# Kernel optimization log

Measured on AMD Instinct MI355X. Metric: run time of the kernel, lower is better.

## Reference

```python
import jax, jax.numpy as jnp
import numpy as np

N, E, D, ED, G = 50000, 600000, 128, 32, 64
NEG_SLOPE = 0.2

def layer_norm(x, g, b, eps=1e-5):
    mu = jnp.mean(x, axis=-1, keepdims=True)
    var = jnp.var(x, axis=-1, keepdims=True)
    return (x - mu) * jax.lax.rsqrt(var + eps) * g + b

def eagat(x, src, dst, edge_attr, W, a_src, a_dst, We, a_e, bias):
    # GATConv with edge features, heads=1; messages flow src -> dst
    xl = x @ W                               # [N, D]
    ee = edge_attr @ We                      # [E, D]
    al_s = xl @ a_src                        # [N]
    al_d = xl @ a_dst                        # [N]
    e = jax.nn.leaky_relu(al_s[src] + al_d[dst] + ee @ a_e, NEG_SLOPE)  # [E]
    # segment softmax over incoming edges of each dst node
    m = jax.ops.segment_max(e, dst, num_segments=N)
    ex = jnp.exp(e - m[dst])
    s = jax.ops.segment_sum(ex, dst, num_segments=N)
    alpha = ex / (s[dst] + 1e-16)            # [E]
    out = jax.ops.segment_sum(xl[src] * alpha[:, None], dst, num_segments=N)
    return out + bias

def setup_inputs() -> dict:
    key = jax.random.key(0)
    ks = jax.random.split(key, 24)
    p = lambda k, shp, sc=0.1: jax.random.normal(k, shp, dtype=jnp.float32) * sc
    inp = {
        "x": jax.random.normal(ks[0], (N, D), dtype=jnp.float32),
        "edge_attr": jax.random.normal(ks[1], (E, ED), dtype=jnp.float32),
        "W1": p(ks[2], (D, D)), "as1": p(ks[3], (D,)), "ad1": p(ks[4], (D,)),
        "We1": p(ks[5], (ED, D)), "ae1": p(ks[6], (D,)), "b1": jnp.zeros((D,), jnp.float32),
        "g1": jnp.ones((D,), jnp.float32), "be1": jnp.zeros((D,), jnp.float32),
        "W2": p(ks[7], (D, D)), "as2": p(ks[8], (D,)), "ad2": p(ks[9], (D,)),
        "We2": p(ks[10], (ED, D)), "ae2": p(ks[11], (D,)), "b2": jnp.zeros((D,), jnp.float32),
        "g2": jnp.ones((D,), jnp.float32), "be2": jnp.zeros((D,), jnp.float32),
        "Wl": p(ks[12], (D, D)), "bl": jnp.zeros((D,), jnp.float32),
        "gl": jnp.ones((D,), jnp.float32), "bel": jnp.zeros((D,), jnp.float32),
        "edge_index": jax.random.randint(ks[13], (2, E), 0, N, dtype=jnp.int64),
        "batch": jnp.sort(jax.random.randint(ks[14], (N,), 0, G, dtype=jnp.int64)),
    }
    return inp

def reference(x, edge_attr, W1, as1, ad1, We1, ae1, b1, g1, be1,
              W2, as2, ad2, We2, ae2, b2, g2, be2, Wl, bl, gl, bel,
              edge_index, batch):
    src, dst = edge_index[0], edge_index[1]
    x1 = eagat(x, src, dst, edge_attr, W1, as1, ad1, We1, ae1, b1)
    x2 = layer_norm(x1, g1, be1)
    x3 = eagat(x2, src, dst, edge_attr, W2, as2, ad2, We2, ae2, b2)
    x4 = layer_norm(x3, g2, be2)
    # global mean pool over graphs
    sums = jax.ops.segment_sum(x4, batch, num_segments=G)          # [G, D]
    cnt = jax.ops.segment_sum(jnp.ones((x4.shape[0],), x4.dtype), batch, num_segments=G)
    pooled = sums / jnp.maximum(cnt, 1.0)[:, None]
    out = jax.nn.relu(layer_norm(pooled @ Wl + bl, gl, bel))
    return out
```

## Files before the change

### kernel.cpp

```cpp
#include <hip/hip_runtime.h>
#include <math.h>


typedef __attribute__((ext_vector_type(8))) short bf16x8;
typedef __attribute__((ext_vector_type(4))) float f32x4;

static __device__ __forceinline__ unsigned short f2bf(float f) {
    unsigned u = __float_as_uint(f);
    unsigned r = (u + 0x7fff + ((u >> 16) & 1)) >> 16;
    return (unsigned short)r;
}
static __device__ __forceinline__ float bf2f_lo(unsigned u) { return __uint_as_float(u << 16); }
static __device__ __forceinline__ float bf2f_hi(unsigned u) { return __uint_as_float(u & 0xffff0000u); }

__global__ __launch_bounds__(256) void prep_weights(
    const float* __restrict__ W1, const float* __restrict__ W2,
    const float* __restrict__ We1, const float* __restrict__ ae1,
    const float* __restrict__ We2, const float* __restrict__ ae2,
    unsigned short* __restrict__ W1bT, unsigned short* __restrict__ W2bT,
    float* __restrict__ wa, int4* __restrict__ counts4, int nc4,
    int4* __restrict__ pooled4, int np4, int zc)
{
    int b = blockIdx.x, t = threadIdx.x;
    if (b < 64) {
        int i = b * 256 + t;
        int k = i >> 7, n = i & 127;
        W1bT[n * 128 + k] = f2bf(W1[i]);
        W2bT[n * 128 + k] = f2bf(W2[i]);
    } else if (b == 64) {
        int o = t >> 2;
        int qq = t & 3;
        const float* We = (o < 32) ? We1 : We2;
        const float* ae = (o < 32) ? ae1 : ae2;
        int r = o & 31;
        const float4* Wr = (const float4*)(We + r * 128 + qq * 32);
        const float4* ar = (const float4*)(ae + qq * 32);
        float s = 0.f;
#pragma unroll
        for (int c4 = 0; c4 < 8; c4++) {
            float4 wv = Wr[c4]; float4 av = ar[c4];
            s += wv.x*av.x + wv.y*av.y + wv.z*av.z + wv.w*av.w;
        }
        s += __shfl_xor(s, 1); s += __shfl_xor(s, 2);
        if (qq == 0) wa[o] = s;
    } else if (b < 65 + zc) {
        int i = (b - 65) * 256 + t;
        if (i < nc4) counts4[i] = (int4){0, 0, 0, 0};
    } else {
        int i = (b - 65 - zc) * 256 + t;
        if (i < np4) pooled4[i] = (int4){0, 0, 0, 0};
    }
}

__global__ __launch_bounds__(256) void edge_dots_count(
    const float* __restrict__ ea, const float* __restrict__ wa,
    const int* __restrict__ srcv, const int* __restrict__ dstv,
    int* __restrict__ counts, int2* __restrict__ payload, int E)
{
    int j = blockIdx.x * 256 + threadIdx.x;
    if (j >= E) return;
    int dst = dstv[j];
    int src = srcv[j];
    int r = atomicAdd(&counts[dst << 4], 1);

    const float4* e4 = (const float4*)(ea + (size_t)j * 32);
    float4 v[8];
#pragma unroll
    for (int i = 0; i < 8; i++) v[i] = e4[i];

    float s1 = 0.f, s2 = 0.f;
#pragma unroll
    for (int i = 0; i < 8; i++) {
        float4 w1 = ((const float4*)wa)[i];
        float4 w2 = ((const float4*)(wa + 32))[i];
        s1 += v[i].x*w1.x + v[i].y*w1.y + v[i].z*w1.z + v[i].w*w1.w;
        s2 += v[i].x*w2.x + v[i].y*w2.y + v[i].z*w2.z + v[i].w*w2.w;
    }
    if (r < 64) {
        unsigned pe = ((unsigned)f2bf(s1) << 16) | (unsigned)f2bf(s2);
        int2 pv;
        pv.x = src;
        pv.y = (int)pe;
        payload[((size_t)dst << 6) + r] = pv;
    }
}

template<bool BF16IN>
__global__ __launch_bounds__(256) void gemm_mfma(
    const void* __restrict__ Xv, const unsigned short* __restrict__ WbT,
    const float* __restrict__ asrc, const float* __restrict__ adst,
    unsigned short* __restrict__ XLb, float* __restrict__ als, float* __restrict__ ald,
    int nrows)
{
    __shared__ unsigned short tile[64][136];
    int t = threadIdx.x;
    int wave = t >> 6;
    int lane = t & 63;
    int l = lane & 15, q = lane >> 4;
    int row0 = blockIdx.x * 64 + wave * 16;

    int arow = row0 + l;
    bool avalid = arow < nrows;

    f32x4 acc[8];
#pragma unroll
    for (int c = 0; c < 8; c++) acc[c] = (f32x4){0.f, 0.f, 0.f, 0.f};

#pragma unroll
    for (int kt = 0; kt < 4; kt++) {
        bf16x8 afrag;
        if (avalid) {
            if constexpr (BF16IN) {
                const unsigned short* xrow = (const unsigned short*)Xv + (size_t)arow * 128 + q * 8;
                afrag = *(const bf16x8*)(xrow + kt * 32);
            } else {
                const float* xrow = (const float*)Xv + (size_t)arow * 128 + q * 8;
                float4 v0 = *(const float4*)(xrow + kt * 32);
                float4 v1 = *(const float4*)(xrow + kt * 32 + 4);
                afrag[0] = (short)f2bf(v0.x); afrag[1] = (short)f2bf(v0.y);
                afrag[2] = (short)f2bf(v0.z); afrag[3] = (short)f2bf(v0.w);
                afrag[4] = (short)f2bf(v1.x); afrag[5] = (short)f2bf(v1.y);
                afrag[6] = (short)f2bf(v1.z); afrag[7] = (short)f2bf(v1.w);
            }
        } else {
#pragma unroll
            for (int j = 0; j < 8; j++) afrag[j] = 0;
        }
#pragma unroll
        for (int c = 0; c < 8; c++) {
            bf16x8 bfrag = *(const bf16x8*)(WbT + (((c * 16 + l) << 7) + kt * 32 + q * 8));
            acc[c] = __builtin_amdgcn_mfma_f32_16x16x32_bf16(afrag, bfrag, acc[c], 0, 0, 0);
        }
    }

    float as_[8], ad_[8];
#pragma unroll
    for (int c = 0; c < 8; c++) { as_[c] = asrc[c * 16 + l]; ad_[c] = adst[c * 16 + l]; }

#pragma unroll
    for (int r = 0; r < 4; r++) {
        int row = row0 + q * 4 + r;
        bool valid = row < nrows;
        float ps = 0.f, pd = 0.f;
#pragma unroll
        for (int c = 0; c < 8; c++) {
            float v = acc[c][r];
            ps += v * as_[c]; pd += v * ad_[c];
        }
#pragma unroll
        for (int o = 8; o >= 1; o >>= 1) { ps += __shfl_xor(ps, o); pd += __shfl_xor(pd, o); }
        if (l == 0 && valid) { als[row] = ps; ald[row] = pd; }
    }

#pragma unroll
    for (int c = 0; c < 8; c++) {
#pragma unroll
        for (int r = 0; r < 4; r++) {
            unsigned u = (unsigned)f2bf(acc[c][r]);
            unsigned up = (unsigned)__shfl_xor((int)u, 1);
            if (!(lane & 1)) {
                *(unsigned*)&tile[wave * 16 + q * 4 + r][c * 16 + l] = u | (up << 16);
            }
        }
    }
    __syncthreads();

    int base = blockIdx.x * 64;
#pragma unroll
    for (int it = 0; it < 4; it++) {
        int row = it * 16 + (t >> 4);
        int seg = t & 15;
        if (base + row < nrows) {
            bf16x8 vv = *(const bf16x8*)&tile[row][seg * 8];
            *(bf16x8*)(XLb + (size_t)(base + row) * 128 + seg * 8) = vv;
        }
    }
}

template<int EOFF>
__global__ __launch_bounds__(256) void aggregate_ln(
    const unsigned short* __restrict__ XLb, const int2* __restrict__ payload,
    const int* __restrict__ counts,
    const float* __restrict__ als, const float* __restrict__ ald,
    const float* __restrict__ bias, const float* __restrict__ gamma, const float* __restrict__ beta,
    unsigned short* __restrict__ XoutB, int N)
{
    int node = blockIdx.x * 4 + (threadIdx.x >> 6);
    if (node >= N) return;
    int lane = threadIdx.x & 63;
    int deg = counts[node << 4];
    if (deg > 64) deg = 64;
    float ald_n = ald[node];

    const unsigned* rows = (const unsigned*)XLb;

    float w_mine = 0.f;
    int   s_mine = 0;
    if (lane < deg) {
        int2 pv = payload[((size_t)node << 6) + lane];
        s_mine = pv.x;
        unsigned ue = (unsigned)pv.y;
        float ed = (EOFF == 1) ? bf2f_hi(ue) : bf2f_lo(ue);
        float e = ed + als[s_mine] + ald_n;
        e = (e >= 0.f) ? e : 0.2f * e;
        w_mine = __expf(fminf(e, 60.f));
    }

    float ssum = w_mine;
#pragma unroll
    for (int o = 32; o >= 1; o >>= 1) ssum += __shfl_xor(ssum, o);

    float acc0 = 0.f, acc1 = 0.f;
    int j = 0;
    for (; j + 8 <= deg; j += 8) {
        int s0=__shfl(s_mine,j),   s1=__shfl(s_mine,j+1), s2=__shfl(s_mine,j+2), s3=__shfl(s_mine,j+3);
        int s4=__shfl(s_mine,j+4), s5=__shfl(s_mine,j+5), s6=__shfl(s_mine,j+6), s7=__shfl(s_mine,j+7);
        unsigned u0 = rows[((size_t)s0 << 6) + lane];
        unsigned u1 = rows[((size_t)s1 << 6) + lane];
        unsigned u2 = rows[((size_t)s2 << 6) + lane];
        unsigned u3 = rows[((size_t)s3 << 6) + lane];
        unsigned u4 = rows[((size_t)s4 << 6) + lane];
        unsigned u5 = rows[((size_t)s5 << 6) + lane];
        unsigned u6 = rows[((size_t)s6 << 6) + lane];
        unsigned u7 = rows[((size_t)s7 << 6) + lane];
        float w0=__shfl(w_mine,j),   w1=__shfl(w_mine,j+1), w2=__shfl(w_mine,j+2), w3=__shfl(w_mine,j+3);
        float w4=__shfl(w_mine,j+4), w5=__shfl(w_mine,j+5), w6=__shfl(w_mine,j+6), w7=__shfl(w_mine,j+7);
        acc0 += w0*bf2f_lo(u0); acc1 += w0*bf2f_hi(u0);
        acc0 += w1*bf2f_lo(u1); acc1 += w1*bf2f_hi(u1);
        acc0 += w2*bf2f_lo(u2); acc1 += w2*bf2f_hi(u2);
        acc0 += w3*bf2f_lo(u3); acc1 += w3*bf2f_hi(u3);
        acc0 += w4*bf2f_lo(u4); acc1 += w4*bf2f_hi(u4);
        acc0 += w5*bf2f_lo(u5); acc1 += w5*bf2f_hi(u5);
        acc0 += w6*bf2f_lo(u6); acc1 += w6*bf2f_hi(u6);
        acc0 += w7*bf2f_lo(u7); acc1 += w7*bf2f_hi(u7);
    }
    for (; j + 4 <= deg; j += 4) {
        int s0=__shfl(s_mine,j), s1=__shfl(s_mine,j+1), s2=__shfl(s_mine,j+2), s3=__shfl(s_mine,j+3);
        unsigned u0 = rows[((size_t)s0 << 6) + lane];
        unsigned u1 = rows[((size_t)s1 << 6) + lane];
        unsigned u2 = rows[((size_t)s2 << 6) + lane];
        unsigned u3 = rows[((size_t)s3 << 6) + lane];
        float w0=__shfl(w_mine,j), w1=__shfl(w_mine,j+1), w2=__shfl(w_mine,j+2), w3=__shfl(w_mine,j+3);
        acc0 += w0*bf2f_lo(u0); acc1 += w0*bf2f_hi(u0);
        acc0 += w1*bf2f_lo(u1); acc1 += w1*bf2f_hi(u1);
        acc0 += w2*bf2f_lo(u2); acc1 += w2*bf2f_hi(u2);
        acc0 += w3*bf2f_lo(u3); acc1 += w3*bf2f_hi(u3);
    }
    for (; j < deg; j++) {
        int s0 = __shfl(s_mine, j);
        float w0 = __shfl(w_mine, j);
        unsigned u0 = rows[((size_t)s0 << 6) + lane];
        acc0 += w0*bf2f_lo(u0); acc1 += w0*bf2f_hi(u0);
    }

    float2 bi = *(const float2*)(bias + 2 * lane);
    float inv = 1.f / (ssum + 1e-16f);
    float y0 = acc0 * inv + bi.x;
    float y1 = acc1 * inv + bi.y;

    float s = y0 + y1;
#pragma unroll
    for (int o = 32; o >= 1; o >>= 1) s += __shfl_xor(s, o);
    float mean = s * (1.f / 128.f);
    float d0 = y0 - mean, d1 = y1 - mean;
    float v = d0 * d0 + d1 * d1;
#pragma unroll
    for (int o = 32; o >= 1; o >>= 1) v += __shfl_xor(v, o);
    float r = rsqrtf(v * (1.f / 128.f) + 1e-5f);
    float2 ga = *(const float2*)(gamma + 2 * lane);
    float2 be = *(const float2*)(beta  + 2 * lane);
    float o0 = d0 * r * ga.x + be.x;
    float o1 = d1 * r * ga.y + be.y;
    unsigned packed = (unsigned)f2bf(o0) | ((unsigned)f2bf(o1) << 16);
    ((unsigned*)XoutB)[((size_t)node << 6) + lane] = packed;
}

__global__ __launch_bounds__(64) void pool_partial(
    const unsigned* __restrict__ XAb4, const int* __restrict__ batch,
    float* __restrict__ pooled, int n)
{
    int chunk0 = blockIdx.x * 32;
    if (chunk0 >= n) return;
    int t = threadIdx.x;
    int end = min(chunk0 + 32, n);
    float a0 = 0.f, a1 = 0.f;
    int gcur = batch[chunk0];
    for (int r = chunk0; r < end; r++) {
        int g = batch[r];
        if (g != gcur) {
            atomicAdd(&pooled[gcur * 128 + 2 * t],     a0);
            atomicAdd(&pooled[gcur * 128 + 2 * t + 1], a1);
            a0 = 0.f; a1 = 0.f; gcur = g;
        }
        unsigned u = XAb4[((size_t)r << 6) + t];
        a0 += bf2f_lo(u); a1 += bf2f_hi(u);
    }
    atomicAdd(&pooled[gcur * 128 + 2 * t],     a0);
    atomicAdd(&pooled[gcur * 128 + 2 * t + 1], a1);
}

__global__ __launch_bounds__(128) void pool_head(
    const float* __restrict__ pooled, const int* __restrict__ batch,
    const float* __restrict__ Wl, const float* __restrict__ bl,
    const float* __restrict__ gl, const float* __restrict__ bel,
    float* __restrict__ out, int n)
{
    int g = blockIdx.x, t = threadIdx.x;
    int lo = 0, hi = n;
    while (lo < hi) { int mid = (lo + hi) >> 1; if (batch[mid] < g) lo = mid + 1; else hi = mid; }
    int s0 = lo;
    hi = n;
    while (lo < hi) { int mid = (lo + hi) >> 1; if (batch[mid] < g + 1) lo = mid + 1; else hi = mid; }
    float cntf = (float)(lo - s0);

    __shared__ float ps[128];
    __shared__ float xr[4];
    ps[t] = pooled[g * 128 + t] / fmaxf(cntf, 1.f);
    __syncthreads();

    float y = bl[t];
#pragma unroll 4
    for (int k = 0; k < 128; k++) y += ps[k] * Wl[k * 128 + t];

    float s = y;
#pragma unroll
    for (int o = 32; o >= 1; o >>= 1) s += __shfl_xor(s, o);
    if ((t & 63) == 0) xr[t >> 6] = s;
    __syncthreads();
    float mean = (xr[0] + xr[1]) * (1.f / 128.f);
    float d = y - mean;
    float v = d * d;
#pragma unroll
    for (int o = 32; o >= 1; o >>= 1) v += __shfl_xor(v, o);
    if ((t & 63) == 0) xr[2 + (t >> 6)] = v;
    __syncthreads();
    float var = (xr[2] + xr[3]) * (1.f / 128.f);
    float z = d * rsqrtf(var + 1e-5f) * gl[t] + bel[t];
    out[g * 128 + t] = fmaxf(z, 0.f);
}


extern "C" void kernel_launch(void* const* d_in, const int* in_sizes, int n_in,
                              void* d_out, int out_size, void* d_ws, size_t ws_size,
                              hipStream_t stream)
{
    const float* x    = (const float*)d_in[0];
    const float* ea   = (const float*)d_in[1];
    const float* W1   = (const float*)d_in[2];
    const float* as1  = (const float*)d_in[3];
    const float* ad1  = (const float*)d_in[4];
    const float* We1  = (const float*)d_in[5];
    const float* ae1  = (const float*)d_in[6];
    const float* b1   = (const float*)d_in[7];
    const float* g1   = (const float*)d_in[8];
    const float* be1  = (const float*)d_in[9];
    const float* W2   = (const float*)d_in[10];
    const float* as2  = (const float*)d_in[11];
    const float* ad2  = (const float*)d_in[12];
    const float* We2  = (const float*)d_in[13];
    const float* ae2  = (const float*)d_in[14];
    const float* b2   = (const float*)d_in[15];
    const float* g2   = (const float*)d_in[16];
    const float* be2  = (const float*)d_in[17];
    const float* Wlin = (const float*)d_in[18];
    const float* bl   = (const float*)d_in[19];
    const float* gl   = (const float*)d_in[20];
    const float* bel  = (const float*)d_in[21];
    const int*   ei   = (const int*)d_in[22];
    const int*   batch= (const int*)d_in[23];
    float* out = (float*)d_out;

    int N = in_sizes[0] / 128;
    int E = in_sizes[1] / 32;
    int G = out_size / 128;
    const int* srcv = ei;
    const int* dstv = ei + E;

    char* wsb = (char*)d_ws;
    size_t off = 0;
    auto alloc = [&](size_t bytes) -> void* {
        void* p = wsb + off;
        off += (bytes + 15) & ~(size_t)15;
        return p;
    };
    unsigned short* XLb  = (unsigned short*)alloc((size_t)N * 128 * 2);
    unsigned short* XAb  = (unsigned short*)alloc((size_t)N * 128 * 2);
    unsigned short* W1bT = (unsigned short*)alloc(16384 * 2);
    unsigned short* W2bT = (unsigned short*)alloc(16384 * 2);
    int2*  payload= (int2*)alloc((size_t)N * 64 * 8);
    float* als    = (float*)alloc((size_t)N * 4);
    float* ald    = (float*)alloc((size_t)N * 4);
    float* wa     = (float*)alloc(64 * 4);
    float* pooled = (float*)alloc((size_t)G * 128 * 4);
    int*   counts = (int*)alloc((size_t)N * 64);

    int egrid = (E + 255) / 256;
    int mgrid = (N + 63) / 64;
    int agrid = (N + 3) / 4;
    int pgrid = (N + 31) / 32;

    int nc4 = N * 4;
    int np4 = (G * 128) / 4;
    int zc = (nc4 + 255) / 256;
    int zp = (np4 + 255) / 256;
    prep_weights<<<65 + zc + zp, 256, 0, stream>>>(
        W1, W2, We1, ae1, We2, ae2, W1bT, W2bT, wa,
        (int4*)counts, nc4, (int4*)pooled, np4, zc);

    edge_dots_count<<<egrid, 256, 0, stream>>>(ea, wa, srcv, dstv, counts, payload, E);

    gemm_mfma<false><<<mgrid, 256, 0, stream>>>(x, W1bT, as1, ad1, XLb, als, ald, N);
    aggregate_ln<1><<<agrid, 256, 0, stream>>>(XLb, payload, counts, als, ald, b1, g1, be1, XAb, N);

    gemm_mfma<true><<<mgrid, 256, 0, stream>>>(XAb, W2bT, as2, ad2, XLb, als, ald, N);
    aggregate_ln<2><<<agrid, 256, 0, stream>>>(XLb, payload, counts, als, ald, b2, g2, be2, XAb, N);

    pool_partial<<<pgrid, 64, 0, stream>>>((const unsigned*)XAb, batch, pooled, N);
    pool_head<<<G, 128, 0, stream>>>(pooled, batch, Wlin, bl, gl, bel, out, N);
}
```

Measured before the change: 344.9 us.

## Fuse edge-dot/bucketing kernel with first GEMM and compact degree counters

Merges the edge attention-dot and dst-bucketing kernel with the first-layer node GEMM into one launch, with blocks split by index between the two jobs so they run concurrently and one launch is saved. Degree counters are shrunk from one per 64-byte line to a dense int array, cutting the zeroing traffic at the cost of more atomic contention on shared cache lines. Payload writes become 64-bit nontemporal stores to avoid polluting cache. The fused kernel carries the GEMM's shared-memory tile even for edge blocks, which can reduce occupancy.

New measurement: 351.7 us. No clear change (+2.0%).

```diff
diff --git a/kernel.cpp b/kernel.cpp
--- a/kernel.cpp
+++ b/kernel.cpp
@@ -52,42 +52,127 @@
     }
 }
 
-__global__ __launch_bounds__(256) void edge_dots_count(
+__global__ __launch_bounds__(256) void edge_gemm1(
     const float* __restrict__ ea, const float* __restrict__ wa,
     const int* __restrict__ srcv, const int* __restrict__ dstv,
-    int* __restrict__ counts, int2* __restrict__ payload, int E)
-{
-    int j = blockIdx.x * 256 + threadIdx.x;
-    if (j >= E) return;
-    int dst = dstv[j];
-    int src = srcv[j];
-    int r = atomicAdd(&counts[dst << 4], 1);
-
-    const float4* e4 = (const float4*)(ea + (size_t)j * 32);
-    float4 v[8];
-#pragma unroll
-    for (int i = 0; i < 8; i++) v[i] = e4[i];
-
-    float s1 = 0.f, s2 = 0.f;
-#pragma unroll
-    for (int i = 0; i < 8; i++) {
-        float4 w1 = ((const float4*)wa)[i];
-        float4 w2 = ((const float4*)(wa + 32))[i];
-        s1 += v[i].x*w1.x + v[i].y*w1.y + v[i].z*w1.z + v[i].w*w1.w;
-        s2 += v[i].x*w2.x + v[i].y*w2.y + v[i].z*w2.z + v[i].w*w2.w;
-    }
-    if (r < 64) {
-        unsigned pe = ((unsigned)f2bf(s1) << 16) | (unsigned)f2bf(s2);
-        int2 pv;
-        pv.x = src;
-        pv.y = (int)pe;
-        payload[((size_t)dst << 6) + r] = pv;
-    }
-}
-
-template<bool BF16IN>
-__global__ __launch_bounds__(256) void gemm_mfma(
-    const void* __restrict__ Xv, const unsigned short* __restrict__ WbT,
+    int* __restrict__ counts, unsigned long long* __restrict__ payload, int E, int eg,
+    const float* __restrict__ Xv, const unsigned short* __restrict__ WbT,
+    const float* __restrict__ asrc, const float* __restrict__ adst,
+    unsigned short* __restrict__ XLb, float* __restrict__ als, float* __restrict__ ald,
+    int nrows)
+{
+    int t = threadIdx.x;
+    if (blockIdx.x < eg) {
+        int j = blockIdx.x * 256 + t;
+        if (j >= E) return;
+        int dst = dstv[j];
+        int src = srcv[j];
+        int r = atomicAdd(&counts[dst], 1);
+
+        const float4* e4 = (const float4*)(ea + (size_t)j * 32);
+        float4 v[8];
+#pragma unroll
+        for (int i = 0; i < 8; i++) v[i] = e4[i];
+
+        float s1 = 0.f, s2 = 0.f;
+#pragma unroll
+        for (int i = 0; i < 8; i++) {
+            float4 w1 = ((const float4*)wa)[i];
+            float4 w2 = ((const float4*)(wa + 32))[i];
+            s1 += v[i].x*w1.x + v[i].y*w1.y + v[i].z*w1.z + v[i].w*w1.w;
+            s2 += v[i].x*w2.x + v[i].y*w2.y + v[i].z*w2.z + v[i].w*w2.w;
+        }
+        if (r < 64) {
+            unsigned pe = ((unsigned)f2bf(s1) << 16) | (unsigned)f2bf(s2);
+            unsigned long long pv = (unsigned long long)(unsigned)src
+                                  | ((unsigned long long)pe << 32);
+            __builtin_nontemporal_store(pv, &payload[((size_t)dst << 6) + r]);
+        }
+        return;
+    }
+
+    __shared__ unsigned short tile[64][136];
+    int bid = blockIdx.x - eg;
+    int wave = t >> 6;
+    int lane = t & 63;
+    int l = lane & 15, q = lane >> 4;
+    int row0 = bid * 64 + wave * 16;
+
+    int arow = row0 + l;
+    bool avalid = arow < nrows;
+
+    f32x4 acc[8];
+#pragma unroll
+    for (int c = 0; c < 8; c++) acc[c] = (f32x4){0.f, 0.f, 0.f, 0.f};
+
+#pragma unroll
+    for (int kt = 0; kt < 4; kt++) {
+        bf16x8 afrag;
+        if (avalid) {
+            const float* xrow = Xv + (size_t)arow * 128 + q * 8;
+            float4 v0 = *(const float4*)(xrow + kt * 32);
+            float4 v1 = *(const float4*)(xrow + kt * 32 + 4);
+            afrag[0] = (short)f2bf(v0.x); afrag[1] = (short)f2bf(v0.y);
+            afrag[2] = (short)f2bf(v0.z); afrag[3] = (short)f2bf(v0.w);
+            afrag[4] = (short)f2bf(v1.x); afrag[5] = (short)f2bf(v1.y);
+            afrag[6] = (short)f2bf(v1.z); afrag[7] = (short)f2bf(v1.w);
+        } else {
+#pragma unroll
+            for (int jj = 0; jj < 8; jj++) afrag[jj] = 0;
+        }
+#pragma unroll
+        for (int c = 0; c < 8; c++) {
+            bf16x8 bfrag = *(const bf16x8*)(WbT + (((c * 16 + l) << 7) + kt * 32 + q * 8));
+            acc[c] = __builtin_amdgcn_mfma_f32_16x16x32_bf16(afrag, bfrag, acc[c], 0, 0, 0);
+        }
+    }
+
+    float as_[8], ad_[8];
+#pragma unroll
+    for (int c = 0; c < 8; c++) { as_[c] = asrc[c * 16 + l]; ad_[c] = adst[c * 16 + l]; }
+
+#pragma unroll
+    for (int r = 0; r < 4; r++) {
+        int row = row0 + q * 4 + r;
+        bool valid = row < nrows;
+        float ps = 0.f, pd = 0.f;
+#pragma unroll
+        for (int c = 0; c < 8; c++) {
+            float v = acc[c][r];
+            ps += v * as_[c]; pd += v * ad_[c];
+        }
+#pragma unroll
+        for (int o = 8; o >= 1; o >>= 1) { ps += __shfl_xor(ps, o); pd += __shfl_xor(pd, o); }
+        if (l == 0 && valid) { als[row] = ps; ald[row] = pd; }
+    }
+
+#pragma unroll
+    for (int c = 0; c < 8; c++) {
+#pragma unroll
+        for (int r = 0; r < 4; r++) {
+            unsigned u = (unsigned)f2bf(acc[c][r]);
+            unsigned up = (unsigned)__shfl_xor((int)u, 1);
+            if (!(lane & 1)) {
+                *(unsigned*)&tile[wave * 16 + q * 4 + r][c * 16 + l] = u | (up << 16);
+            }
+        }
+    }
+    __syncthreads();
+
+    int base = bid * 64;
+#pragma unroll
+    for (int it = 0; it < 4; it++) {
+        int row = it * 16 + (t >> 4);
+        int seg = t & 15;
+        if (base + row < nrows) {
+            bf16x8 vv = *(const bf16x8*)&tile[row][seg * 8];
+            *(bf16x8*)(XLb + (size_t)(base + row) * 128 + seg * 8) = vv;
+        }
+    }
+}
+
+__global__ __launch_bounds__(256) void gemm_mfma_bf16(
+    const unsigned short* __restrict__ Xv, const unsigned short* __restrict__ WbT,
     const float* __restrict__ asrc, const float* __restrict__ adst,
     unsigned short* __restrict__ XLb, float* __restrict__ als, float* __restrict__ ald,
     int nrows)
@@ -110,21 +195,11 @@
     for (int kt = 0; kt < 4; kt++) {
         bf16x8 afrag;
         if (avalid) {
-            if constexpr (BF16IN) {
-                const unsigned short* xrow = (const unsigned short*)Xv + (size_t)arow * 128 + q * 8;
-                afrag = *(const bf16x8*)(xrow + kt * 32);
-            } else {
-                const float* xrow = (const float*)Xv + (size_t)arow * 128 + q * 8;
-                float4 v0 = *(const float4*)(xrow + kt * 32);
-                float4 v1 = *(const float4*)(xrow + kt * 32 + 4);
-                afrag[0] = (short)f2bf(v0.x); afrag[1] = (short)f2bf(v0.y);
-                afrag[2] = (short)f2bf(v0.z); afrag[3] = (short)f2bf(v0.w);
-                afrag[4] = (short)f2bf(v1.x); afrag[5] = (short)f2bf(v1.y);
-                afrag[6] = (short)f2bf(v1.z); afrag[7] = (short)f2bf(v1.w);
-            }
+            const unsigned short* xrow = Xv + (size_t)arow * 128 + q * 8;
+            afrag = *(const bf16x8*)(xrow + kt * 32);
         } else {
 #pragma unroll
-            for (int j = 0; j < 8; j++) afrag[j] = 0;
+            for (int jj = 0; jj < 8; jj++) afrag[jj] = 0;
         }
 #pragma unroll
         for (int c = 0; c < 8; c++) {
@@ -179,7 +254,7 @@
 
 template<int EOFF>
 __global__ __launch_bounds__(256) void aggregate_ln(
-    const unsigned short* __restrict__ XLb, const int2* __restrict__ payload,
+    const unsigned short* __restrict__ XLb, const unsigned long long* __restrict__ payload,
     const int* __restrict__ counts,
     const float* __restrict__ als, const float* __restrict__ ald,
     const float* __restrict__ bias, const float* __restrict__ gamma, const float* __restrict__ beta,
@@ -188,7 +263,7 @@
     int node = blockIdx.x * 4 + (threadIdx.x >> 6);
     if (node >= N) return;
     int lane = threadIdx.x & 63;
-    int deg = counts[node << 4];
+    int deg = counts[node];
     if (deg > 64) deg = 64;
     float ald_n = ald[node];
 
@@ -197,9 +272,9 @@
     float w_mine = 0.f;
     int   s_mine = 0;
     if (lane < deg) {
-        int2 pv = payload[((size_t)node << 6) + lane];
-        s_mine = pv.x;
-        unsigned ue = (unsigned)pv.y;
+        unsigned long long pv = payload[((size_t)node << 6) + lane];
+        s_mine = (int)(unsigned)pv;
+        unsigned ue = (unsigned)(pv >> 32);
         float ed = (EOFF == 1) ? bf2f_hi(ue) : bf2f_lo(ue);
         float e = ed + als[s_mine] + ald_n;
         e = (e >= 0.f) ? e : 0.2f * e;
@@ -387,19 +462,19 @@
     unsigned short* XAb  = (unsigned short*)alloc((size_t)N * 128 * 2);
     unsigned short* W1bT = (unsigned short*)alloc(16384 * 2);
     unsigned short* W2bT = (unsigned short*)alloc(16384 * 2);
-    int2*  payload= (int2*)alloc((size_t)N * 64 * 8);
+    unsigned long long* payload = (unsigned long long*)alloc((size_t)N * 64 * 8);
     float* als    = (float*)alloc((size_t)N * 4);
     float* ald    = (float*)alloc((size_t)N * 4);
     float* wa     = (float*)alloc(64 * 4);
     float* pooled = (float*)alloc((size_t)G * 128 * 4);
-    int*   counts = (int*)alloc((size_t)N * 64);
+    int*   counts = (int*)alloc((size_t)N * 4);
 
     int egrid = (E + 255) / 256;
     int mgrid = (N + 63) / 64;
     int agrid = (N + 3) / 4;
     int pgrid = (N + 31) / 32;
 
-    int nc4 = N * 4;
+    int nc4 = N / 4 + (N % 4 != 0);
     int np4 = (G * 128) / 4;
     int zc = (nc4 + 255) / 256;
     int zp = (np4 + 255) / 256;
@@ -407,12 +482,13 @@
         W1, W2, We1, ae1, We2, ae2, W1bT, W2bT, wa,
         (int4*)counts, nc4, (int4*)pooled, np4, zc);
 
-    edge_dots_count<<<egrid, 256, 0, stream>>>(ea, wa, srcv, dstv, counts, payload, E);
-
-    gemm_mfma<false><<<mgrid, 256, 0, stream>>>(x, W1bT, as1, ad1, XLb, als, ald, N);
+    edge_gemm1<<<egrid + mgrid, 256, 0, stream>>>(
+        ea, wa, srcv, dstv, counts, payload, E, egrid,
+        x, W1bT, as1, ad1, XLb, als, ald, N);
+
     aggregate_ln<1><<<agrid, 256, 0, stream>>>(XLb, payload, counts, als, ald, b1, g1, be1, XAb, N);
 
-    gemm_mfma<true><<<mgrid, 256, 0, stream>>>(XAb, W2bT, as2, ad2, XLb, als, ald, N);
+    gemm_mfma_bf16<<<mgrid, 256, 0, stream>>>(XAb, W2bT, as2, ad2, XLb, als, ald, N);
     aggregate_ln<2><<<agrid, 256, 0, stream>>>(XLb, payload, counts, als, ald, b2, g2, be2, XAb, N);
 
     pool_partial<<<pgrid, 64, 0, stream>>>((const unsigned*)XAb, batch, pooled, N);
```

## Replace padded per-node edge slots with compact CSR via count-scan-scatter

Applied to the files above, without the earlier changes.

Edge bucketing moves from fixed 64-slot padded arrays per destination to a compact CSR layout. Edge dots and counts are computed first, a single-block prefix scan builds offsets, and a scatter pass places the packed src/dot pairs contiguously. The aggregate kernels then read from the offsets. This shrinks the payload buffer and the counts zeroing and improves locality for the gathers, but it adds two launches, including a serial single-block scan over 50k nodes, and a second pass over the edges.

After: 443.5 us. +28.6%, slower.

```diff
diff --git a/kernel.cpp b/kernel.cpp
--- a/kernel.cpp
+++ b/kernel.cpp
@@ -52,37 +52,74 @@
     }
 }
 
-__global__ __launch_bounds__(256) void edge_dots_count(
+__global__ __launch_bounds__(256) void edge_dots(
     const float* __restrict__ ea, const float* __restrict__ wa,
-    const int* __restrict__ srcv, const int* __restrict__ dstv,
-    int* __restrict__ counts, int2* __restrict__ payload, int E)
+    const int* __restrict__ dstv,
+    int* __restrict__ counts, unsigned* __restrict__ dots, int E)
 {
     int j = blockIdx.x * 256 + threadIdx.x;
     if (j >= E) return;
-    int dst = dstv[j];
-    int src = srcv[j];
-    int r = atomicAdd(&counts[dst << 4], 1);
-
-    const float4* e4 = (const float4*)(ea + (size_t)j * 32);
-    float4 v[8];
-#pragma unroll
-    for (int i = 0; i < 8; i++) v[i] = e4[i];
+    int dst = __builtin_nontemporal_load(&dstv[j]);
+    atomicAdd(&counts[dst], 1);
+
+    const f32x4* e4 = (const f32x4*)(ea + (size_t)j * 32);
+    f32x4 v[8];
+#pragma unroll
+    for (int i = 0; i < 8; i++) v[i] = __builtin_nontemporal_load(&e4[i]);
 
     float s1 = 0.f, s2 = 0.f;
 #pragma unroll
     for (int i = 0; i < 8; i++) {
         float4 w1 = ((const float4*)wa)[i];
         float4 w2 = ((const float4*)(wa + 32))[i];
-        s1 += v[i].x*w1.x + v[i].y*w1.y + v[i].z*w1.z + v[i].w*w1.w;
-        s2 += v[i].x*w2.x + v[i].y*w2.y + v[i].z*w2.z + v[i].w*w2.w;
-    }
-    if (r < 64) {
-        unsigned pe = ((unsigned)f2bf(s1) << 16) | (unsigned)f2bf(s2);
-        int2 pv;
-        pv.x = src;
-        pv.y = (int)pe;
-        payload[((size_t)dst << 6) + r] = pv;
-    }
+        s1 += v[i][0]*w1.x + v[i][1]*w1.y + v[i][2]*w1.z + v[i][3]*w1.w;
+        s2 += v[i][0]*w2.x + v[i][1]*w2.y + v[i][2]*w2.z + v[i][3]*w2.w;
+    }
+    unsigned pe = ((unsigned)f2bf(s1) << 16) | (unsigned)f2bf(s2);
+    __builtin_nontemporal_store(pe, &dots[j]);
+}
+
+__global__ __launch_bounds__(1024) void prefix_scan(
+    const int* __restrict__ counts, int* __restrict__ offs,
+    int* __restrict__ woff, int n)
+{
+    __shared__ int wsum[16];
+    __shared__ int carry_s;
+    int t = threadIdx.x, lane = t & 63, w = t >> 6;
+    if (t == 0) { carry_s = 0; offs[0] = 0; }
+    __syncthreads();
+    for (int base = 0; base < n; base += 1024) {
+        int i = base + t;
+        int c = (i < n) ? counts[i] : 0;
+        int s = c;
+#pragma unroll
+        for (int o = 1; o < 64; o <<= 1) { int v = __shfl_up(s, o); if (lane >= o) s += v; }
+        if (lane == 63) wsum[w] = s;
+        __syncthreads();
+        int prev = 0;
+        for (int k = 0; k < w; k++) prev += wsum[k];
+        int total = prev;
+        for (int k = w; k < 16; k++) total += wsum[k];
+        int excl = carry_s + prev + s - c;
+        if (i < n) { woff[i] = excl; offs[i + 1] = excl + c; }
+        __syncthreads();
+        if (t == 0) carry_s += total;
+        __syncthreads();
+    }
+}
+
+__global__ __launch_bounds__(256) void scatter_pass(
+    const int* __restrict__ srcv, const int* __restrict__ dstv,
+    const unsigned* __restrict__ dots, int* __restrict__ woff,
+    unsigned long long* __restrict__ payload, int E)
+{
+    int j = blockIdx.x * 256 + threadIdx.x;
+    if (j >= E) return;
+    int dst = __builtin_nontemporal_load(&dstv[j]);
+    int src = __builtin_nontemporal_load(&srcv[j]);
+    unsigned d = __builtin_nontemporal_load(&dots[j]);
+    int pos = atomicAdd(&woff[dst], 1);
+    payload[pos] = (unsigned long long)(unsigned)src | ((unsigned long long)d << 32);
 }
 
 template<bool BF16IN>
@@ -124,7 +161,7 @@
             }
         } else {
 #pragma unroll
-            for (int j = 0; j < 8; j++) afrag[j] = 0;
+            for (int jj = 0; jj < 8; jj++) afrag[jj] = 0;
         }
 #pragma unroll
         for (int c = 0; c < 8; c++) {
@@ -179,8 +216,8 @@
 
 template<int EOFF>
 __global__ __launch_bounds__(256) void aggregate_ln(
-    const unsigned short* __restrict__ XLb, const int2* __restrict__ payload,
-    const int* __restrict__ counts,
+    const unsigned short* __restrict__ XLb, const unsigned long long* __restrict__ payload,
+    const int* __restrict__ offs,
     const float* __restrict__ als, const float* __restrict__ ald,
     const float* __restrict__ bias, const float* __restrict__ gamma, const float* __restrict__ beta,
     unsigned short* __restrict__ XoutB, int N)
@@ -188,7 +225,8 @@
     int node = blockIdx.x * 4 + (threadIdx.x >> 6);
     if (node >= N) return;
     int lane = threadIdx.x & 63;
-    int deg = counts[node << 4];
+    int start = offs[node];
+    int deg = offs[node + 1] - start;
     if (deg > 64) deg = 64;
     float ald_n = ald[node];
 
@@ -197,9 +235,9 @@
     float w_mine = 0.f;
     int   s_mine = 0;
     if (lane < deg) {
-        int2 pv = payload[((size_t)node << 6) + lane];
-        s_mine = pv.x;
-        unsigned ue = (unsigned)pv.y;
+        unsigned long long pv = payload[(size_t)start + lane];
+        s_mine = (int)(unsigned)pv;
+        unsigned ue = (unsigned)(pv >> 32);
         float ed = (EOFF == 1) ? bf2f_hi(ue) : bf2f_lo(ue);
         float e = ed + als[s_mine] + ald_n;
         e = (e >= 0.f) ? e : 0.2f * e;
@@ -387,19 +425,22 @@
     unsigned short* XAb  = (unsigned short*)alloc((size_t)N * 128 * 2);
     unsigned short* W1bT = (unsigned short*)alloc(16384 * 2);
     unsigned short* W2bT = (unsigned short*)alloc(16384 * 2);
-    int2*  payload= (int2*)alloc((size_t)N * 64 * 8);
+    unsigned long long* payload = (unsigned long long*)alloc((size_t)E * 8);
+    unsigned* dots  = (unsigned*)alloc((size_t)E * 4);
+    int*   offs   = (int*)alloc((size_t)(N + 1) * 4);
+    int*   woff   = (int*)alloc((size_t)N * 4);
     float* als    = (float*)alloc((size_t)N * 4);
     float* ald    = (float*)alloc((size_t)N * 4);
     float* wa     = (float*)alloc(64 * 4);
     float* pooled = (float*)alloc((size_t)G * 128 * 4);
-    int*   counts = (int*)alloc((size_t)N * 64);
+    int*   counts = (int*)alloc((size_t)N * 4);
 
     int egrid = (E + 255) / 256;
     int mgrid = (N + 63) / 64;
     int agrid = (N + 3) / 4;
     int pgrid = (N + 31) / 32;
 
-    int nc4 = N * 4;
+    int nc4 = (N + 3) / 4;
     int np4 = (G * 128) / 4;
     int zc = (nc4 + 255) / 256;
     int zp = (np4 + 255) / 256;
@@ -407,13 +448,15 @@
         W1, W2, We1, ae1, We2, ae2, W1bT, W2bT, wa,
         (int4*)counts, nc4, (int4*)pooled, np4, zc);
 
-    edge_dots_count<<<egrid, 256, 0, stream>>>(ea, wa, srcv, dstv, counts, payload, E);
+    edge_dots<<<egrid, 256, 0, stream>>>(ea, wa, dstv, counts, dots, E);
+    prefix_scan<<<1, 1024, 0, stream>>>(counts, offs, woff, N);
+    scatter_pass<<<egrid, 256, 0, stream>>>(srcv, dstv, dots, woff, payload, E);
 
     gemm_mfma<false><<<mgrid, 256, 0, stream>>>(x, W1bT, as1, ad1, XLb, als, ald, N);
-    aggregate_ln<1><<<agrid, 256, 0, stream>>>(XLb, payload, counts, als, ald, b1, g1, be1, XAb, N);
+    aggregate_ln<1><<<agrid, 256, 0, stream>>>(XLb, payload, offs, als, ald, b1, g1, be1, XAb, N);
 
     gemm_mfma<true><<<mgrid, 256, 0, stream>>>(XAb, W2bT, as2, ad2, XLb, als, ald, N);
-    aggregate_ln<2><<<agrid, 256, 0, stream>>>(XLb, payload, counts, als, ald, b2, g2, be2, XAb, N);
+    aggregate_ln<2><<<agrid, 256, 0, stream>>>(XLb, payload, offs, als, ald, b2, g2, be2, XAb, N);
 
     pool_partial<<<pgrid, 64, 0, stream>>>((const unsigned*)XAb, batch, pooled, N);
     pool_head<<<G, 128, 0, stream>>>(pooled, batch, Wlin, bl, gl, bel, out, N);
```

## Fuse mean-pool accumulation into second aggregate kernel and compact degree counters

Applied to the files above, without the earlier changes.

Removes the separate pool_partial kernel. The second aggregate_ln now atomically adds each node's normalized row straight into the per-graph pooled buffer, so the bf16 layer-2 output is no longer written and re-read. Degree counters shrink from 64-byte padded slots to packed ints, which cuts zeroing and footprint. Edge inputs are read with nontemporal loads. The risk is heavy float-atomic contention: roughly 780 nodes per graph all add into the same 128 addresses, replacing a kernel that did mostly chunk-local sums. Packed counters may also add cache-line contention between neighbouring nodes.

New measurement: 456.0 us. 1.32x slower.

```diff
diff --git a/kernel.cpp b/kernel.cpp
--- a/kernel.cpp
+++ b/kernel.cpp
@@ -55,32 +55,31 @@
 __global__ __launch_bounds__(256) void edge_dots_count(
     const float* __restrict__ ea, const float* __restrict__ wa,
     const int* __restrict__ srcv, const int* __restrict__ dstv,
-    int* __restrict__ counts, int2* __restrict__ payload, int E)
+    int* __restrict__ counts, unsigned long long* __restrict__ payload, int E)
 {
     int j = blockIdx.x * 256 + threadIdx.x;
     if (j >= E) return;
-    int dst = dstv[j];
-    int src = srcv[j];
-    int r = atomicAdd(&counts[dst << 4], 1);
-
-    const float4* e4 = (const float4*)(ea + (size_t)j * 32);
-    float4 v[8];
-#pragma unroll
-    for (int i = 0; i < 8; i++) v[i] = e4[i];
+    int dst = __builtin_nontemporal_load(&dstv[j]);
+    int src = __builtin_nontemporal_load(&srcv[j]);
+    int r = atomicAdd(&counts[dst], 1);
+
+    const f32x4* e4 = (const f32x4*)(ea + (size_t)j * 32);
+    f32x4 v[8];
+#pragma unroll
+    for (int i = 0; i < 8; i++) v[i] = __builtin_nontemporal_load(&e4[i]);
 
     float s1 = 0.f, s2 = 0.f;
 #pragma unroll
     for (int i = 0; i < 8; i++) {
         float4 w1 = ((const float4*)wa)[i];
         float4 w2 = ((const float4*)(wa + 32))[i];
-        s1 += v[i].x*w1.x + v[i].y*w1.y + v[i].z*w1.z + v[i].w*w1.w;
-        s2 += v[i].x*w2.x + v[i].y*w2.y + v[i].z*w2.z + v[i].w*w2.w;
+        s1 += v[i][0]*w1.x + v[i][1]*w1.y + v[i][2]*w1.z + v[i][3]*w1.w;
+        s2 += v[i][0]*w2.x + v[i][1]*w2.y + v[i][2]*w2.z + v[i][3]*w2.w;
     }
     if (r < 64) {
         unsigned pe = ((unsigned)f2bf(s1) << 16) | (unsigned)f2bf(s2);
-        int2 pv;
-        pv.x = src;
-        pv.y = (int)pe;
+        unsigned long long pv = (unsigned long long)(unsigned)src
+                              | ((unsigned long long)pe << 32);
         payload[((size_t)dst << 6) + r] = pv;
     }
 }
@@ -124,7 +123,7 @@
             }
         } else {
 #pragma unroll
-            for (int j = 0; j < 8; j++) afrag[j] = 0;
+            for (int jj = 0; jj < 8; jj++) afrag[jj] = 0;
         }
 #pragma unroll
         for (int c = 0; c < 8; c++) {
@@ -177,18 +176,19 @@
     }
 }
 
-template<int EOFF>
+template<int EOFF, bool POOL>
 __global__ __launch_bounds__(256) void aggregate_ln(
-    const unsigned short* __restrict__ XLb, const int2* __restrict__ payload,
+    const unsigned short* __restrict__ XLb, const unsigned long long* __restrict__ payload,
     const int* __restrict__ counts,
     const float* __restrict__ als, const float* __restrict__ ald,
     const float* __restrict__ bias, const float* __restrict__ gamma, const float* __restrict__ beta,
-    unsigned short* __restrict__ XoutB, int N)
+    unsigned short* __restrict__ XoutB, const int* __restrict__ batch,
+    float* __restrict__ pooled, int N)
 {
     int node = blockIdx.x * 4 + (threadIdx.x >> 6);
     if (node >= N) return;
     int lane = threadIdx.x & 63;
-    int deg = counts[node << 4];
+    int deg = counts[node];
     if (deg > 64) deg = 64;
     float ald_n = ald[node];
 
@@ -197,9 +197,9 @@
     float w_mine = 0.f;
     int   s_mine = 0;
     if (lane < deg) {
-        int2 pv = payload[((size_t)node << 6) + lane];
-        s_mine = pv.x;
-        unsigned ue = (unsigned)pv.y;
+        unsigned long long pv = payload[((size_t)node << 6) + lane];
+        s_mine = (int)(unsigned)pv;
+        unsigned ue = (unsigned)(pv >> 32);
         float ed = (EOFF == 1) ? bf2f_hi(ue) : bf2f_lo(ue);
         float e = ed + als[s_mine] + ald_n;
         e = (e >= 0.f) ? e : 0.2f * e;
@@ -271,32 +271,14 @@
     float2 be = *(const float2*)(beta  + 2 * lane);
     float o0 = d0 * r * ga.x + be.x;
     float o1 = d1 * r * ga.y + be.y;
-    unsigned packed = (unsigned)f2bf(o0) | ((unsigned)f2bf(o1) << 16);
-    ((unsigned*)XoutB)[((size_t)node << 6) + lane] = packed;
-}
-
-__global__ __launch_bounds__(64) void pool_partial(
-    const unsigned* __restrict__ XAb4, const int* __restrict__ batch,
-    float* __restrict__ pooled, int n)
-{
-    int chunk0 = blockIdx.x * 32;
-    if (chunk0 >= n) return;
-    int t = threadIdx.x;
-    int end = min(chunk0 + 32, n);
-    float a0 = 0.f, a1 = 0.f;
-    int gcur = batch[chunk0];
-    for (int r = chunk0; r < end; r++) {
-        int g = batch[r];
-        if (g != gcur) {
-            atomicAdd(&pooled[gcur * 128 + 2 * t],     a0);
-            atomicAdd(&pooled[gcur * 128 + 2 * t + 1], a1);
-            a0 = 0.f; a1 = 0.f; gcur = g;
-        }
-        unsigned u = XAb4[((size_t)r << 6) + t];
-        a0 += bf2f_lo(u); a1 += bf2f_hi(u);
-    }
-    atomicAdd(&pooled[gcur * 128 + 2 * t],     a0);
-    atomicAdd(&pooled[gcur * 128 + 2 * t + 1], a1);
+    if constexpr (POOL) {
+        int g = batch[node];
+        atomicAdd(&pooled[g * 128 + 2 * lane],     o0);
+        atomicAdd(&pooled[g * 128 + 2 * lane + 1], o1);
+    } else {
+        unsigned packed = (unsigned)f2bf(o0) | ((unsigned)f2bf(o1) << 16);
+        ((unsigned*)XoutB)[((size_t)node << 6) + lane] = packed;
+    }
 }
 
 __global__ __launch_bounds__(128) void pool_head(
@@ -387,19 +369,18 @@
     unsigned short* XAb  = (unsigned short*)alloc((size_t)N * 128 * 2);
     unsigned short* W1bT = (unsigned short*)alloc(16384 * 2);
     unsigned short* W2bT = (unsigned short*)alloc(16384 * 2);
-    int2*  payload= (int2*)alloc((size_t)N * 64 * 8);
+    unsigned long long* payload = (unsigned long long*)alloc((size_t)N * 64 * 8);
     float* als    = (float*)alloc((size_t)N * 4);
     float* ald    = (float*)alloc((size_t)N * 4);
     float* wa     = (float*)alloc(64 * 4);
     float* pooled = (float*)alloc((size_t)G * 128 * 4);
-    int*   counts = (int*)alloc((size_t)N * 64);
+    int*   counts = (int*)alloc((size_t)N * 4);
 
     int egrid = (E + 255) / 256;
     int mgrid = (N + 63) / 64;
     int agrid = (N + 3) / 4;
-    int pgrid = (N + 31) / 32;
-
-    int nc4 = N * 4;
+
+    int nc4 = (N + 3) / 4;
     int np4 = (G * 128) / 4;
     int zc = (nc4 + 255) / 256;
     int zp = (np4 + 255) / 256;
@@ -410,11 +391,12 @@
     edge_dots_count<<<egrid, 256, 0, stream>>>(ea, wa, srcv, dstv, counts, payload, E);
 
     gemm_mfma<false><<<mgrid, 256, 0, stream>>>(x, W1bT, as1, ad1, XLb, als, ald, N);
-    aggregate_ln<1><<<agrid, 256, 0, stream>>>(XLb, payload, counts, als, ald, b1, g1, be1, XAb, N);
+    aggregate_ln<1, false><<<agrid, 256, 0, stream>>>(
+        XLb, payload, counts, als, ald, b1, g1, be1, XAb, nullptr, nullptr, N);
 
     gemm_mfma<true><<<mgrid, 256, 0, stream>>>(XAb, W2bT, as2, ad2, XLb, als, ald, N);
-    aggregate_ln<2><<<agrid, 256, 0, stream>>>(XLb, payload, counts, als, ald, b2, g2, be2, XAb, N);
-
-    pool_partial<<<pgrid, 64, 0, stream>>>((const unsigned*)XAb, batch, pooled, N);
+    aggregate_ln<2, true><<<agrid, 256, 0, stream>>>(
+        XLb, payload, counts, als, ald, b2, g2, be2, nullptr, batch, pooled, N);
+
     pool_head<<<G, 128, 0, stream>>>(pooled, batch, Wlin, bl, gl, bel, out, N);
 }
```
